# Performance work log

Hardware: AMD Instinct MI355X
Metric: run time of the kernel (lower is better)

The kernel has to match this reference:

```python
import jax, jax.numpy as jnp
import numpy as np

N_EMBD = 2048
EPS = 1e-5

def layernorm(x, g, b):
    mu = jnp.mean(x, axis=-1, keepdims=True)
    var = jnp.mean(jnp.square(x - mu), axis=-1, keepdims=True)
    return (x - mu) * jax.lax.rsqrt(var + EPS) * g + b

def gelu_erf(x):
    return x * 0.5 * (1.0 + jax.lax.erf(x / jnp.sqrt(jnp.asarray(2.0, x.dtype))))

def setup_inputs() -> dict:
    key = jax.random.key(0)
    ks = jax.random.split(key, 2)
    x = jax.random.normal(ks[0], (4, 4096, N_EMBD), dtype=jnp.float32)
    W = jax.random.normal(ks[1], (N_EMBD, N_EMBD), dtype=jnp.float32) / np.sqrt(N_EMBD)
    bW = jnp.zeros((N_EMBD,), jnp.float32)
    g1 = jnp.ones((N_EMBD,), jnp.float32)
    b1 = jnp.zeros((N_EMBD,), jnp.float32)
    g2 = jnp.ones((N_EMBD,), jnp.float32)
    b2 = jnp.zeros((N_EMBD,), jnp.float32)
    return {"x": x, "W": W, "bW": bW, "g1": g1, "b1": b1, "g2": g2, "b2": b2}

def reference(x, W, bW, g1, b1, g2, b2):
    h = layernorm(x, g1, b1)                         # [B,S,D]
    h = jnp.einsum('bsd,ed->bse', h, W) + bW         # Linear(D,D)
    h = gelu_erf(h)
    return layernorm(h, g2, b2)
```

## Files before the change

### kernel.cpp

```cpp
#include <hip/hip_runtime.h>
#include <hip/hip_bf16.h>
#include <math.h>


#define D 2048
#define MROWS 16384
#define BMT 256
#define BNT 256
#define NS 64

typedef __bf16 bf16x8 __attribute__((ext_vector_type(8)));
typedef float f32x4 __attribute__((ext_vector_type(4)));

#define GLP(p) ((const __attribute__((address_space(1))) void*)(p))
#define LDSP(p) ((__attribute__((address_space(3))) void*)(p))
#define S_VMCNT(n) asm volatile("s_waitcnt vmcnt(" #n ")" ::: "memory")
#define BAR() __builtin_amdgcn_s_barrier()
#define SCHED_FENCE() __builtin_amdgcn_sched_barrier(0)

__device__ __forceinline__ float gelu_f(float v) {
  return 0.5f * v * (1.0f + erff(v * 0.70710678118654752f));
}

__global__ __launch_bounds__(256) void ln1_kernel(
    const float* __restrict__ x, const float* __restrict__ g,
    const float* __restrict__ b, __hip_bfloat16* __restrict__ out) {
  const int tid = threadIdx.x;
  const size_t row = blockIdx.x;
  const float4* xr = (const float4*)(x + row * D);
  float4 v0 = xr[2 * tid];
  float4 v1 = xr[2 * tid + 1];
  float s  = v0.x + v0.y + v0.z + v0.w + v1.x + v1.y + v1.z + v1.w;
  float ss = v0.x*v0.x + v0.y*v0.y + v0.z*v0.z + v0.w*v0.w
           + v1.x*v1.x + v1.y*v1.y + v1.z*v1.z + v1.w*v1.w;
#pragma unroll
  for (int off = 32; off > 0; off >>= 1) {
    s  += __shfl_down(s, off, 64);
    ss += __shfl_down(ss, off, 64);
  }
  __shared__ float red[8];
  const int w = tid >> 6;
  if ((tid & 63) == 0) { red[w] = s; red[w + 4] = ss; }
  __syncthreads();
  s  = red[0] + red[1] + red[2] + red[3];
  ss = red[4] + red[5] + red[6] + red[7];
  const float mu  = s * (1.0f / D);
  const float var = ss * (1.0f / D) - mu * mu;
  const float inv = rsqrtf(var + 1e-5f);
  const float4* gv = (const float4*)g;
  const float4* bv = (const float4*)b;
  float4 g0 = gv[2 * tid], g1 = gv[2 * tid + 1];
  float4 b0 = bv[2 * tid], b1 = bv[2 * tid + 1];
  alignas(16) __hip_bfloat16 h[8];
  h[0] = __float2bfloat16((v0.x - mu) * inv * g0.x + b0.x);
  h[1] = __float2bfloat16((v0.y - mu) * inv * g0.y + b0.y);
  h[2] = __float2bfloat16((v0.z - mu) * inv * g0.z + b0.z);
  h[3] = __float2bfloat16((v0.w - mu) * inv * g0.w + b0.w);
  h[4] = __float2bfloat16((v1.x - mu) * inv * g1.x + b1.x);
  h[5] = __float2bfloat16((v1.y - mu) * inv * g1.y + b1.y);
  h[6] = __float2bfloat16((v1.z - mu) * inv * g1.z + b1.z);
  h[7] = __float2bfloat16((v1.w - mu) * inv * g1.w + b1.w);
  *(uint4*)(out + row * D + (size_t)tid * 8) = *(const uint4*)h;
}

__global__ __launch_bounds__(256) void cvt_kernel(
    const float* __restrict__ W, __hip_bfloat16* __restrict__ Wb, int n8) {
  const int i = blockIdx.x * 256 + threadIdx.x;
  if (i >= n8) return;
  const float4* p = (const float4*)W + 2 * (size_t)i;
  float4 a = p[0], c = p[1];
  alignas(16) __hip_bfloat16 h[8] = {
      __float2bfloat16(a.x), __float2bfloat16(a.y),
      __float2bfloat16(a.z), __float2bfloat16(a.w),
      __float2bfloat16(c.x), __float2bfloat16(c.y),
      __float2bfloat16(c.z), __float2bfloat16(c.w)};
  *(uint4*)(Wb + (size_t)i * 8) = *(const uint4*)h;
}

__global__ __launch_bounds__(512, 2) void gemm_kernel(
    const __hip_bfloat16* __restrict__ A,
    const __hip_bfloat16* __restrict__ Bw,
    const float* __restrict__ bias,
    float* __restrict__ C) {
  __shared__ __hip_bfloat16 sA[4 * 8192];
  __shared__ __hip_bfloat16 sB[4 * 8192];
  const int tid = threadIdx.x;
  const int l = tid & 63;
  const int wid = tid >> 6;
  const int fr = l & 15;
  const int lk = l >> 4;

  const int nid = blockIdx.x;
  const int xk = nid & 7, j = nid >> 3;
  const int bx = (xk << 3) | (j >> 3);
  const int by = j & 7;
  const size_t m0 = (size_t)bx * BMT;
  const int n0 = by * BNT;

  const int whm = wid >> 2;
  const int wn = (wid & 3) * 64;

  const int srow = ((tid >> 6) << 4) + (tid & 15);
  const int scol = ((tid >> 4) & 3) * 8;
  const int ldd = tid * 16;
  const __hip_bfloat16* const Ag = A + m0 * D + (size_t)srow * D + scol;
  const __hip_bfloat16* const Bg = Bw + (size_t)n0 * D + (size_t)srow * D + scol;

  auto stgA = [&](int s) {
    const int ro = (s & 3) << 14;
    __builtin_amdgcn_global_load_lds(GLP(Ag + s * 32), LDSP((char*)sA + ro + ldd), 16, 0, 0);
    __builtin_amdgcn_global_load_lds(GLP(Ag + (size_t)128 * D + s * 32), LDSP((char*)sA + ro + 8192 + ldd), 16, 0, 0);
  };
  auto stgB = [&](int s) {
    const int ro = (s & 3) << 14;
    __builtin_amdgcn_global_load_lds(GLP(Bg + s * 32), LDSP((char*)sB + ro + ldd), 16, 0, 0);
    __builtin_amdgcn_global_load_lds(GLP(Bg + (size_t)128 * D + s * 32), LDSP((char*)sB + ro + 8192 + ldd), 16, 0, 0);
  };

  const int abase = whm * 8192 + l * 16;
  const int bbase = (wid & 3) * 4096 + l * 16;

  bf16x8 a[8], b[4];
  f32x4 acc[8][4] = {};

  auto rdA = [&](int s) {
    const char* pa = (const char*)sA + ((s & 3) << 14) + abase;
#pragma unroll
    for (int mi = 0; mi < 8; ++mi) a[mi] = *(const bf16x8*)(pa + mi * 1024);
  };
  auto rdB = [&](int s) {
    const char* pb = (const char*)sB + ((s & 3) << 14) + bbase;
#pragma unroll
    for (int ni = 0; ni < 4; ++ni) b[ni] = *(const bf16x8*)(pb + ni * 1024);
  };
  auto mma32 = [&]() {
    __builtin_amdgcn_s_setprio(1);
#pragma unroll
    for (int mi = 0; mi < 8; ++mi)
#pragma unroll
      for (int ni = 0; ni < 4; ++ni)
        acc[mi][ni] = __builtin_amdgcn_mfma_f32_16x16x32_bf16(a[mi], b[ni], acc[mi][ni], 0, 0, 0);
    __builtin_amdgcn_s_setprio(0);
  };

  stgA(0); stgB(0); stgA(1); stgB(1); stgA(2); stgB(2);

  for (int s = 0; s < NS; ++s) {
    if (s <= 61) { S_VMCNT(8); }
    else if (s == 62) { S_VMCNT(4); }
    else { S_VMCNT(0); }
    BAR(); SCHED_FENCE();
    rdA(s); rdB(s);
    if (s < 61) { stgA(s + 3); stgB(s + 3); }
    mma32();
  }

  float bv[4];
#pragma unroll
  for (int ni = 0; ni < 4; ++ni) bv[ni] = bias[n0 + wn + ni * 16 + fr];
#pragma unroll
  for (int mi = 0; mi < 8; ++mi) {
    const size_t rbase = m0 + whm * 128 + mi * 16 + lk * 4;
#pragma unroll
    for (int rr = 0; rr < 4; ++rr) {
      float* crow = C + (rbase + rr) * D + n0 + wn + fr;
#pragma unroll
      for (int ni = 0; ni < 4; ++ni)
        crow[ni * 16] = gelu_f(acc[mi][ni][rr] + bv[ni]);
    }
  }
}

__global__ __launch_bounds__(256) void ln2_kernel(
    float* __restrict__ C, const float* __restrict__ g, const float* __restrict__ b) {
  const int tid = threadIdx.x;
  const size_t row = blockIdx.x;
  float4* cr = (float4*)(C + row * D);
  float4 v0 = cr[2 * tid], v1 = cr[2 * tid + 1];
  float s  = v0.x + v0.y + v0.z + v0.w + v1.x + v1.y + v1.z + v1.w;
  float ss = v0.x*v0.x + v0.y*v0.y + v0.z*v0.z + v0.w*v0.w
           + v1.x*v1.x + v1.y*v1.y + v1.z*v1.z + v1.w*v1.w;
#pragma unroll
  for (int off = 32; off > 0; off >>= 1) {
    s  += __shfl_down(s, off, 64);
    ss += __shfl_down(ss, off, 64);
  }
  __shared__ float red[8];
  const int w = tid >> 6;
  if ((tid & 63) == 0) { red[w] = s; red[w + 4] = ss; }
  __syncthreads();
  s  = red[0] + red[1] + red[2] + red[3];
  ss = red[4] + red[5] + red[6] + red[7];
  const float mu  = s * (1.0f / D);
  const float var = ss * (1.0f / D) - mu * mu;
  const float inv = rsqrtf(var + 1e-5f);
  const float4* gv = (const float4*)g;
  const float4* bv = (const float4*)b;
  float4 g0 = gv[2 * tid], g1 = gv[2 * tid + 1];
  float4 b0 = bv[2 * tid], b1 = bv[2 * tid + 1];
  float4 o0, o1;
  o0.x = (v0.x - mu) * inv * g0.x + b0.x;
  o0.y = (v0.y - mu) * inv * g0.y + b0.y;
  o0.z = (v0.z - mu) * inv * g0.z + b0.z;
  o0.w = (v0.w - mu) * inv * g0.w + b0.w;
  o1.x = (v1.x - mu) * inv * g1.x + b1.x;
  o1.y = (v1.y - mu) * inv * g1.y + b1.y;
  o1.z = (v1.z - mu) * inv * g1.z + b1.z;
  o1.w = (v1.w - mu) * inv * g1.w + b1.w;
  cr[2 * tid] = o0;
  cr[2 * tid + 1] = o1;
}

extern "C" void kernel_launch(void* const* d_in, const int* in_sizes, int n_in,
                              void* d_out, int out_size, void* d_ws, size_t ws_size,
                              hipStream_t stream) {
  const float* x  = (const float*)d_in[0];
  const float* W  = (const float*)d_in[1];
  const float* bW = (const float*)d_in[2];
  const float* g1 = (const float*)d_in[3];
  const float* b1 = (const float*)d_in[4];
  const float* g2 = (const float*)d_in[5];
  const float* b2 = (const float*)d_in[6];
  float* out = (float*)d_out;

  __hip_bfloat16* Abf = (__hip_bfloat16*)d_ws;
  __hip_bfloat16* Wbf = Abf + (size_t)MROWS * D;

  ln1_kernel<<<MROWS, 256, 0, stream>>>(x, g1, b1, Abf);
  cvt_kernel<<<(D * D / 8) / 256, 256, 0, stream>>>(W, Wbf, D * D / 8);
  gemm_kernel<<<(MROWS / BMT) * (D / BNT), 512, 0, stream>>>(Abf, Wbf, bW, out);
  ln2_kernel<<<MROWS, 256, 0, stream>>>(out, g2, b2);
}
```

Baseline: 246.6 us.

## Load A fragments directly from global into registers, shrink GEMM tile to 256x128

The GEMM no longer stages A through LDS. Each wave loads its A fragments straight from global memory into double-buffered registers (even/odd), while only B goes through a 4-stage LDS ring. The block shrinks to 256 threads with a 256x128 tile, and the XCD-aware block swizzle is replaced by a simple row-major mapping. This removes LDS traffic and space for A, at the cost of less coalesced global loads for A, less B reuse per block, and lost L2 locality from dropping the swizzle.

Result: slower. 412.7 us (+67.3%).

```diff
diff --git a/kernel.cpp b/kernel.cpp
--- a/kernel.cpp
+++ b/kernel.cpp
@@ -6,7 +6,7 @@
 #define D 2048
 #define MROWS 16384
 #define BMT 256
-#define BNT 256
+#define BNT 128
 #define NS 64
 
 typedef __bf16 bf16x8 __attribute__((ext_vector_type(8)));
@@ -77,83 +77,90 @@
   *(uint4*)(Wb + (size_t)i * 8) = *(const uint4*)h;
 }
 
-__global__ __launch_bounds__(512, 2) void gemm_kernel(
+__global__ __launch_bounds__(256, 2) void gemm_kernel(
     const __hip_bfloat16* __restrict__ A,
     const __hip_bfloat16* __restrict__ Bw,
     const float* __restrict__ bias,
     float* __restrict__ C) {
-  __shared__ __hip_bfloat16 sA[4 * 8192];
-  __shared__ __hip_bfloat16 sB[4 * 8192];
+  __shared__ __hip_bfloat16 sB[4 * 4096];
   const int tid = threadIdx.x;
   const int l = tid & 63;
   const int wid = tid >> 6;
   const int fr = l & 15;
   const int lk = l >> 4;
-
-  const int nid = blockIdx.x;
-  const int xk = nid & 7, j = nid >> 3;
-  const int bx = (xk << 3) | (j >> 3);
-  const int by = j & 7;
+  const int bx = blockIdx.x >> 4;
+  const int by = blockIdx.x & 15;
   const size_t m0 = (size_t)bx * BMT;
   const int n0 = by * BNT;
-
-  const int whm = wid >> 2;
-  const int wn = (wid & 3) * 64;
-
-  const int srow = ((tid >> 6) << 4) + (tid & 15);
+  const int whm = wid >> 1;
+  const int wn = (wid & 1) * 64;
+
+  const int srow = (tid >> 6) * 16 + (tid & 15);
   const int scol = ((tid >> 4) & 3) * 8;
   const int ldd = tid * 16;
-  const __hip_bfloat16* const Ag = A + m0 * D + (size_t)srow * D + scol;
-  const __hip_bfloat16* const Bg = Bw + (size_t)n0 * D + (size_t)srow * D + scol;
-
-  auto stgA = [&](int s) {
-    const int ro = (s & 3) << 14;
-    __builtin_amdgcn_global_load_lds(GLP(Ag + s * 32), LDSP((char*)sA + ro + ldd), 16, 0, 0);
-    __builtin_amdgcn_global_load_lds(GLP(Ag + (size_t)128 * D + s * 32), LDSP((char*)sA + ro + 8192 + ldd), 16, 0, 0);
-  };
+  const __hip_bfloat16* const Bg = Bw + ((size_t)n0 + srow) * D + scol;
+
   auto stgB = [&](int s) {
-    const int ro = (s & 3) << 14;
+    const int ro = (s & 3) << 13;
     __builtin_amdgcn_global_load_lds(GLP(Bg + s * 32), LDSP((char*)sB + ro + ldd), 16, 0, 0);
-    __builtin_amdgcn_global_load_lds(GLP(Bg + (size_t)128 * D + s * 32), LDSP((char*)sB + ro + 8192 + ldd), 16, 0, 0);
-  };
-
-  const int abase = whm * 8192 + l * 16;
-  const int bbase = (wid & 3) * 4096 + l * 16;
-
-  bf16x8 a[8], b[4];
+    __builtin_amdgcn_global_load_lds(GLP(Bg + (size_t)64 * D + s * 32), LDSP((char*)sB + ro + 4096 + ldd), 16, 0, 0);
+  };
+
+  const __hip_bfloat16* const Ag = A + (m0 + (size_t)whm * 128 + fr) * D + lk * 8;
+
+  bf16x8 aE[8], aO[8], b[4];
   f32x4 acc[8][4] = {};
 
-  auto rdA = [&](int s) {
-    const char* pa = (const char*)sA + ((s & 3) << 14) + abase;
-#pragma unroll
-    for (int mi = 0; mi < 8; ++mi) a[mi] = *(const bf16x8*)(pa + mi * 1024);
-  };
+  auto ldA = [&](int s, bf16x8* ar) {
+#pragma unroll
+    for (int mi = 0; mi < 8; ++mi)
+      ar[mi] = *(const bf16x8*)(Ag + (size_t)mi * 16 * D + s * 32);
+  };
+  const int bbase = (wid & 1) * 4096 + l * 16;
   auto rdB = [&](int s) {
-    const char* pb = (const char*)sB + ((s & 3) << 14) + bbase;
+    const char* pb = (const char*)sB + ((s & 3) << 13) + bbase;
 #pragma unroll
     for (int ni = 0; ni < 4; ++ni) b[ni] = *(const bf16x8*)(pb + ni * 1024);
   };
-  auto mma32 = [&]() {
+  auto mma32 = [&](const bf16x8* ar) {
     __builtin_amdgcn_s_setprio(1);
 #pragma unroll
     for (int mi = 0; mi < 8; ++mi)
 #pragma unroll
       for (int ni = 0; ni < 4; ++ni)
-        acc[mi][ni] = __builtin_amdgcn_mfma_f32_16x16x32_bf16(a[mi], b[ni], acc[mi][ni], 0, 0, 0);
+        acc[mi][ni] = __builtin_amdgcn_mfma_f32_16x16x32_bf16(ar[mi], b[ni], acc[mi][ni], 0, 0, 0);
     __builtin_amdgcn_s_setprio(0);
   };
 
-  stgA(0); stgB(0); stgA(1); stgB(1); stgA(2); stgB(2);
-
-  for (int s = 0; s < NS; ++s) {
-    if (s <= 61) { S_VMCNT(8); }
-    else if (s == 62) { S_VMCNT(4); }
-    else { S_VMCNT(0); }
+  stgB(0); stgB(1); ldA(0, aE); stgB(2);
+
+  for (int sp = 0; sp < 30; ++sp) {
+    const int s = 2 * sp;
+    S_VMCNT(4);
     BAR(); SCHED_FENCE();
-    rdA(s); rdB(s);
-    if (s < 61) { stgA(s + 3); stgB(s + 3); }
-    mma32();
-  }
+    rdB(s); ldA(s + 1, aO); stgB(s + 3);
+    mma32(aE);
+    S_VMCNT(4);
+    BAR(); SCHED_FENCE();
+    rdB(s + 1); ldA(s + 2, aE); stgB(s + 4);
+    mma32(aO);
+  }
+  S_VMCNT(4);
+  BAR(); SCHED_FENCE();
+  rdB(60); ldA(61, aO); stgB(63);
+  mma32(aE);
+  S_VMCNT(4);
+  BAR(); SCHED_FENCE();
+  rdB(61); ldA(62, aE);
+  mma32(aO);
+  S_VMCNT(0);
+  BAR(); SCHED_FENCE();
+  rdB(62); ldA(63, aO);
+  mma32(aE);
+  S_VMCNT(0);
+  BAR(); SCHED_FENCE();
+  rdB(63);
+  mma32(aO);
 
   float bv[4];
 #pragma unroll
@@ -228,6 +235,6 @@
 
   ln1_kernel<<<MROWS, 256, 0, stream>>>(x, g1, b1, Abf);
   cvt_kernel<<<(D * D / 8) / 256, 256, 0, stream>>>(W, Wbf, D * D / 8);
-  gemm_kernel<<<(MROWS / BMT) * (D / BNT), 512, 0, stream>>>(Abf, Wbf, bW, out);
+  gemm_kernel<<<(MROWS / BMT) * (D / BNT), 256, 0, stream>>>(Abf, Wbf, bW, out);
   ln2_kernel<<<MROWS, 256, 0, stream>>>(out, g2, b2);
 }
```
